# Optimization experiments

Measured on AMD Instinct MI355X. Metric: run time of the kernel, lower is better.

The kernel has to match this reference:

```python
import jax, jax.numpy as jnp
import numpy as np
from itertools import combinations_with_replacement

LATENT_DIM = 16
N_PARAMS = 2
N_VARS = LATENT_DIM + N_PARAMS  # 18
POLY_ORDER = 3
BATCH = 131072

# Static exponent index tables: for each degree d, an [n_terms_d, d] array of
# variable indices (combinations with replacement), matching a sympy-style
# polynomial library [1, x_i, x_i*x_j, x_i*x_j*x_k, ...].
IDX = [np.array(list(combinations_with_replacement(range(N_VARS), d)), dtype=np.int32)
       for d in range(1, POLY_ORDER + 1)]
P = 1 + sum(a.shape[0] for a in IDX)  # 1330 library terms


def setup_inputs() -> dict:
    key = jax.random.key(0)
    k1, k2, k3 = jax.random.split(key, 3)
    z = jax.random.normal(k1, (BATCH, LATENT_DIM), dtype=jnp.float32)
    betas = jax.random.normal(k2, (BATCH, N_PARAMS), dtype=jnp.float32)
    big_xi = jax.random.normal(k3, (P, N_VARS), dtype=jnp.float32) * 0.1
    mask = jnp.ones((P, N_VARS), dtype=jnp.float32)
    return {"z": z, "betas": betas, "big_xi": big_xi, "mask": mask}


def _theta(x):
    # x: [B, N_VARS] -> theta: [B, P]
    cols = [jnp.ones((x.shape[0], 1), dtype=x.dtype)]  # constant term
    for idx in IDX:
        acc = x[:, idx[:, 0]]                # [B, n_terms_d]
        for k in range(1, idx.shape[1]):     # loop over degree (<= POLY_ORDER)
            acc = acc * x[:, idx[:, k]]
        cols.append(acc)
    return jnp.concatenate(cols, axis=1)


def reference(z, betas, big_xi, mask):
    x = jnp.concatenate([z, betas], axis=1)  # [B, N_VARS]
    theta = _theta(x)                        # [B, P]
    return theta @ (big_xi * mask)           # [B, N_VARS]
```

## Files before the change

### kernel.cpp

```cpp
#include <hip/hip_runtime.h>
#include <hip/hip_bf16.h>
#include <utility>


constexpr int NVARS   = 18;
constexpr int NOUT    = 18;
constexpr int NROWS   = 131072;
constexpr int PTERMS  = 1330;
constexpr int NCHUNKS = 43;
constexpr int NSLOTS  = NCHUNKS * 8;

constexpr int WF0_SHORTS = NCHUNKS * 512;
constexpr int WF1_SHORTS = NCHUNKS * 64;
constexpr int WF_SHORTS  = WF0_SHORTS + WF1_SHORTS;

typedef __attribute__((ext_vector_type(8))) short short8;
typedef __attribute__((ext_vector_type(4))) float f32x4;

struct T3 { int a, b, c; };

constexpr int rho1(int v) {
    if (v < 16)  return (v & ~3) | ((v + 1) & 3);
    if (v == 16) return 17;
    if (v == 17) return 16;
    return v;
}
constexpr int rho2v(int v) { return rho1(rho1(v)); }

constexpr T3 sort3(int u0, int u1, int u2) {
    int t = 0;
    if (u0 > u1) { t = u0; u0 = u1; u1 = t; }
    if (u1 > u2) { t = u1; u1 = u2; u2 = t; }
    if (u0 > u1) { t = u0; u0 = u1; u1 = t; }
    return T3{u0, u1, u2};
}
constexpr T3 rho3(T3 t) { return sort3(rho1(t.a), rho1(t.b), rho1(t.c)); }

constexpr bool t3_less(T3 x, T3 y) {
    if (x.a != y.a) return x.a < y.a;
    if (x.b != y.b) return x.b < y.b;
    return x.c < y.c;
}
constexpr bool t3_eq(T3 x, T3 y) { return x.a == y.a && x.b == y.b && x.c == y.c; }

constexpr int rank_of(T3 t) {
    int deg = (t.a < 18) + (t.b < 18) + (t.c < 18);
    if (deg == 0) return 0;
    if (deg == 1) return 1 + t.a;
    if (deg == 2) {
        int r = 19;
        for (int a = 0; a < t.a; ++a) r += 18 - a;
        return r + (t.b - t.a);
    }
    int r = 190;
    for (int a = 0; a < t.a; ++a) { int n = 18 - a; r += n * (n + 1) / 2; }
    for (int b = t.a; b < t.b; ++b) r += 18 - b;
    return r + (t.c - t.b);
}

struct RepTables {
    signed char va[NSLOTS], vb[NSLOTS], vc[NSLOTS];
    short p[4][NSLOTS];
    int count;
};

constexpr void consider(RepTables& R, int& s, T3 t) {
    T3 im[4] = {t, T3{0, 0, 0}, T3{0, 0, 0}, T3{0, 0, 0}};
    im[1] = rho3(im[0]);
    im[2] = rho3(im[1]);
    im[3] = rho3(im[2]);
    for (int g = 1; g < 4; ++g)
        if (t3_less(im[g], t)) return;
    R.va[s] = (signed char)t.a; R.vb[s] = (signed char)t.b; R.vc[s] = (signed char)t.c;
    for (int g = 0; g < 4; ++g) {
        bool dup = false;
        for (int h = 0; h < g; ++h)
            if (t3_eq(im[h], im[g])) dup = true;
        R.p[g][s] = dup ? (short)-1 : (short)rank_of(im[g]);
    }
    ++s;
}

constexpr RepTables make_tables() {
    RepTables R{};
    int s = 0;
    consider(R, s, T3{18, 18, 18});
    for (int a = 0; a < NVARS; ++a) consider(R, s, T3{a, 18, 18});
    for (int a = 0; a < NVARS; ++a)
        for (int b = a; b < NVARS; ++b) consider(R, s, T3{a, b, 18});
    for (int a = 0; a < NVARS; ++a)
        for (int b = a; b < NVARS; ++b)
            for (int c = b; c < NVARS; ++c) consider(R, s, T3{a, b, c});
    R.count = s;
    for (; s < NSLOTS; ++s) {
        R.va[s] = 19; R.vb[s] = 19; R.vc[s] = 19;
        for (int g = 0; g < 4; ++g) R.p[g][s] = -1;
    }
    return R;
}

constexpr RepTables h_tab = make_tables();
static_assert(h_tab.count == 342, "orbit enumeration must give 342 rep slots");
__device__ const RepTables d_tab = make_tables();


#if __has_builtin(__builtin_amdgcn_cvt_pk_bf16_f32)
typedef __bf16 bf16x2 __attribute__((ext_vector_type(2)));
__device__ __forceinline__ unsigned pack2(float f0, float f1) {
    bf16x2 r = __builtin_amdgcn_cvt_pk_bf16_f32(f0, f1);
    return __builtin_bit_cast(unsigned, r);
}
#else
__device__ __forceinline__ unsigned pack2(float f0, float f1) {
    unsigned u0 = __float_as_uint(f0) + 0x8000u;
    unsigned u1 = __float_as_uint(f1) + 0x8000u;
    return __builtin_amdgcn_perm(u1, u0, 0x07060302u);
}
#endif


template <int S>
__device__ __forceinline__ float term_val(const float (&x)[NVARS]) {
    constexpr int a = h_tab.va[S], b = h_tab.vb[S], c = h_tab.vc[S];
    if constexpr (a >= 19)      return 0.0f;
    else if constexpr (a == 18) return 1.0f;
    else if constexpr (b == 18) return x[a];
    else if constexpr (c == 18) return x[a] * x[b];
    else                        return x[a] * x[b] * x[c];
}

union AFrag { unsigned u[4]; short8 v; };
union BFrag { unsigned u[4]; short8 v; };

template <int CI, int... I>
__device__ __forceinline__ void eval8(const float (&x)[NVARS], float (&t)[8],
                                      std::integer_sequence<int, I...>) {
    ((t[I] = term_val<CI * 8 + I>(x)), ...);
}

template <int CI>
__device__ __forceinline__ void kstep(const float (&xA)[NVARS], const float (&xB)[NVARS],
                                      const short* p0, const short* p1, unsigned zmask,
                                      f32x4& acc00, f32x4& acc01,
                                      f32x4& acc10, f32x4& acc11) {
    float tA[8], tB[8];
    eval8<CI>(xA, tA, std::make_integer_sequence<int, 8>{});
    eval8<CI>(xB, tB, std::make_integer_sequence<int, 8>{});
    AFrag afA, afB;
#pragma unroll
    for (int j = 0; j < 4; ++j) {
        afA.u[j] = pack2(tA[2 * j], tA[2 * j + 1]);
        afB.u[j] = pack2(tB[2 * j], tB[2 * j + 1]);
    }
    short8 b0 = *(const short8*)(p0 + CI * 512);
    BFrag b1;
    b1.v = *(const short8*)(p1 + CI * 64);
#pragma unroll
    for (int j = 0; j < 4; ++j) b1.u[j] &= zmask;
    acc00 = __builtin_amdgcn_mfma_f32_16x16x32_bf16(afA.v, b0,   acc00, 0, 0, 0);
    acc10 = __builtin_amdgcn_mfma_f32_16x16x32_bf16(afB.v, b0,   acc10, 0, 0, 0);
    acc01 = __builtin_amdgcn_mfma_f32_16x16x32_bf16(afA.v, b1.v, acc01, 0, 0, 0);
    acc11 = __builtin_amdgcn_mfma_f32_16x16x32_bf16(afB.v, b1.v, acc11, 0, 0, 0);
}

template <int... CI>
__device__ __forceinline__ void kloop(const float (&xA)[NVARS], const float (&xB)[NVARS],
                                      const short* p0, const short* p1, unsigned zmask,
                                      f32x4& acc00, f32x4& acc01,
                                      f32x4& acc10, f32x4& acc11,
                                      std::integer_sequence<int, CI...>) {
    (kstep<CI>(xA, xB, p0, p1, zmask, acc00, acc01, acc10, acc11), ...);
}

__device__ __forceinline__ void load_x(const float* __restrict__ z,
                                       const float* __restrict__ betas,
                                       int arow, bool s1, bool s2, float (&x)[NVARS]) {
    float x0[NVARS];
    const float4* z4 = (const float4*)(z + (size_t)arow * 16);
    float4 v0 = z4[0], v1 = z4[1], v2 = z4[2], v3 = z4[3];
    x0[0]  = v0.x; x0[1]  = v0.y; x0[2]  = v0.z; x0[3]  = v0.w;
    x0[4]  = v1.x; x0[5]  = v1.y; x0[6]  = v1.z; x0[7]  = v1.w;
    x0[8]  = v2.x; x0[9]  = v2.y; x0[10] = v2.z; x0[11] = v2.w;
    x0[12] = v3.x; x0[13] = v3.y; x0[14] = v3.z; x0[15] = v3.w;
    const float2 b2 = *(const float2*)(betas + (size_t)arow * 2);
    x0[16] = b2.x; x0[17] = b2.y;
    float y[NVARS];
#pragma unroll
    for (int v = 0; v < NVARS; ++v) y[v] = s1 ? x0[rho1(v)] : x0[v];
#pragma unroll
    for (int v = 0; v < NVARS; ++v) x[v] = s2 ? y[rho2v(v)] : y[v];
}

__global__ __launch_bounds__(256, 4) void vindy_mfma(const float* __restrict__ z,
                                                     const float* __restrict__ betas,
                                                     const short* __restrict__ wf,
                                                     float* __restrict__ out) {
    __shared__ __align__(16) short ldsW[WF_SHORTS];
    {
        const float4* src = (const float4*)wf;
        float4* dst = (float4*)ldsW;
        for (int i = threadIdx.x; i < WF_SHORTS / 8; i += 256) dst[i] = src[i];
    }
    __syncthreads();

    const int lane = threadIdx.x & 63;
    const int wave = threadIdx.x >> 6;
    const int g    = lane >> 4;
    const int n    = lane & 15;
    const int rowbase = blockIdx.x * 128 + wave * 32;

    const bool s1 = (g & 1) != 0;
    const bool s2 = (g & 2) != 0;
    float xA[NVARS], xB[NVARS];
    load_x(z, betas, rowbase + n,      s1, s2, xA);
    load_x(z, betas, rowbase + 16 + n, s1, s2, xB);

    const unsigned zmask = (n < 2) ? 0xFFFFFFFFu : 0u;
    const short* p0 = ldsW + lane * 8;
    const short* p1 = ldsW + WF0_SHORTS + (g * 2 + (n < 2 ? n : 0)) * 8;

    f32x4 acc00, acc01, acc10, acc11;
#pragma unroll
    for (int i = 0; i < 4; ++i) { acc00[i] = 0.0f; acc01[i] = 0.0f; acc10[i] = 0.0f; acc11[i] = 0.0f; }

    kloop(xA, xB, p0, p1, zmask, acc00, acc01, acc10, acc11,
          std::make_integer_sequence<int, NCHUNKS>{});

    float* o0 = out + (size_t)(rowbase + g * 4) * NOUT;
    float* o1 = out + (size_t)(rowbase + 16 + g * 4) * NOUT;
#pragma unroll
    for (int r = 0; r < 4; ++r) {
        o0[(size_t)r * NOUT + n] = acc00[r];
        o1[(size_t)r * NOUT + n] = acc10[r];
    }
    if (n < 2) {
#pragma unroll
        for (int r = 0; r < 4; ++r) {
            o0[(size_t)r * NOUT + 16 + n] = acc01[r];
            o1[(size_t)r * NOUT + 16 + n] = acc11[r];
        }
    }
}


__global__ void prep_wfrag(const float* __restrict__ xi, const float* __restrict__ mask,
                           __hip_bfloat16* __restrict__ wf) {
    int i = blockIdx.x * blockDim.x + threadIdx.x;
    if (i >= WF_SHORTS) return;
    int p = -1, col = 0;
    if (i < WF0_SHORTS) {
        int j = i & 7, l = (i >> 3) & 63, c = i >> 9;
        col = l & 15;
        p = d_tab.p[l >> 4][c * 8 + j];
    } else {
        int i2 = i - WF0_SHORTS;
        int j = i2 & 7, q = (i2 >> 3) & 7, c = i2 >> 6;
        col = 16 + (q & 1);
        p = d_tab.p[q >> 1][c * 8 + j];
    }
    float v = 0.0f;
    if (p >= 0) v = xi[p * NOUT + col] * mask[p * NOUT + col];
    wf[i] = __float2bfloat16(v);
}

extern "C" void kernel_launch(void* const* d_in, const int* in_sizes, int n_in,
                              void* d_out, int out_size, void* d_ws, size_t ws_size,
                              hipStream_t stream) {
    const float* z     = (const float*)d_in[0];
    const float* betas = (const float*)d_in[1];
    const float* xi    = (const float*)d_in[2];
    const float* mask  = (const float*)d_in[3];
    __hip_bfloat16* wf = (__hip_bfloat16*)d_ws;
    float* out = (float*)d_out;

    prep_wfrag<<<(WF_SHORTS + 255) / 256, 256, 0, stream>>>(xi, mask, wf);
    vindy_mfma<<<NROWS / 128, 256, 0, stream>>>(z, betas, (const short*)d_ws, out);
}
```

Baseline: 90.45 us.

## Use 1024-thread blocks and zero-padded B1 fragment slots instead of masking

Measured after the change: 96.91 us. +7.1%, slower.

```diff
diff --git a/kernel.cpp b/kernel.cpp
--- a/kernel.cpp
+++ b/kernel.cpp
@@ -11,7 +11,7 @@
 constexpr int NSLOTS  = NCHUNKS * 8;
 
 constexpr int WF0_SHORTS = NCHUNKS * 512;
-constexpr int WF1_SHORTS = NCHUNKS * 64;
+constexpr int WF1_SHORTS = NCHUNKS * 12 * 8;
 constexpr int WF_SHORTS  = WF0_SHORTS + WF1_SHORTS;
 
 typedef __attribute__((ext_vector_type(8))) short short8;
@@ -130,7 +130,6 @@
 }
 
 union AFrag { unsigned u[4]; short8 v; };
-union BFrag { unsigned u[4]; short8 v; };
 
 template <int CI, int... I>
 __device__ __forceinline__ void eval8(const float (&x)[NVARS], float (&t)[8],
@@ -140,7 +139,7 @@
 
 template <int CI>
 __device__ __forceinline__ void kstep(const float (&xA)[NVARS], const float (&xB)[NVARS],
-                                      const short* p0, const short* p1, unsigned zmask,
+                                      const short* p0, const short* p1,
                                       f32x4& acc00, f32x4& acc01,
                                       f32x4& acc10, f32x4& acc11) {
     float tA[8], tB[8];
@@ -153,23 +152,20 @@
         afB.u[j] = pack2(tB[2 * j], tB[2 * j + 1]);
     }
     short8 b0 = *(const short8*)(p0 + CI * 512);
-    BFrag b1;
-    b1.v = *(const short8*)(p1 + CI * 64);
-#pragma unroll
-    for (int j = 0; j < 4; ++j) b1.u[j] &= zmask;
-    acc00 = __builtin_amdgcn_mfma_f32_16x16x32_bf16(afA.v, b0,   acc00, 0, 0, 0);
-    acc10 = __builtin_amdgcn_mfma_f32_16x16x32_bf16(afB.v, b0,   acc10, 0, 0, 0);
-    acc01 = __builtin_amdgcn_mfma_f32_16x16x32_bf16(afA.v, b1.v, acc01, 0, 0, 0);
-    acc11 = __builtin_amdgcn_mfma_f32_16x16x32_bf16(afB.v, b1.v, acc11, 0, 0, 0);
+    short8 b1 = *(const short8*)(p1 + CI * (12 * 8));
+    acc00 = __builtin_amdgcn_mfma_f32_16x16x32_bf16(afA.v, b0, acc00, 0, 0, 0);
+    acc10 = __builtin_amdgcn_mfma_f32_16x16x32_bf16(afB.v, b0, acc10, 0, 0, 0);
+    acc01 = __builtin_amdgcn_mfma_f32_16x16x32_bf16(afA.v, b1, acc01, 0, 0, 0);
+    acc11 = __builtin_amdgcn_mfma_f32_16x16x32_bf16(afB.v, b1, acc11, 0, 0, 0);
 }
 
 template <int... CI>
 __device__ __forceinline__ void kloop(const float (&xA)[NVARS], const float (&xB)[NVARS],
-                                      const short* p0, const short* p1, unsigned zmask,
+                                      const short* p0, const short* p1,
                                       f32x4& acc00, f32x4& acc01,
                                       f32x4& acc10, f32x4& acc11,
                                       std::integer_sequence<int, CI...>) {
-    (kstep<CI>(xA, xB, p0, p1, zmask, acc00, acc01, acc10, acc11), ...);
+    (kstep<CI>(xA, xB, p0, p1, acc00, acc01, acc10, acc11), ...);
 }
 
 __device__ __forceinline__ void load_x(const float* __restrict__ z,
@@ -191,15 +187,15 @@
     for (int v = 0; v < NVARS; ++v) x[v] = s2 ? y[rho2v(v)] : y[v];
 }
 
-__global__ __launch_bounds__(256, 4) void vindy_mfma(const float* __restrict__ z,
-                                                     const float* __restrict__ betas,
-                                                     const short* __restrict__ wf,
-                                                     float* __restrict__ out) {
+__global__ __launch_bounds__(1024, 4) void vindy_mfma(const float* __restrict__ z,
+                                                      const float* __restrict__ betas,
+                                                      const short* __restrict__ wf,
+                                                      float* __restrict__ out) {
     __shared__ __align__(16) short ldsW[WF_SHORTS];
     {
         const float4* src = (const float4*)wf;
         float4* dst = (float4*)ldsW;
-        for (int i = threadIdx.x; i < WF_SHORTS / 8; i += 256) dst[i] = src[i];
+        for (int i = threadIdx.x; i < WF_SHORTS / 8; i += 1024) dst[i] = src[i];
     }
     __syncthreads();
 
@@ -207,7 +203,7 @@
     const int wave = threadIdx.x >> 6;
     const int g    = lane >> 4;
     const int n    = lane & 15;
-    const int rowbase = blockIdx.x * 128 + wave * 32;
+    const int rowbase = blockIdx.x * 512 + wave * 32;
 
     const bool s1 = (g & 1) != 0;
     const bool s2 = (g & 2) != 0;
@@ -215,15 +211,14 @@
     load_x(z, betas, rowbase + n,      s1, s2, xA);
     load_x(z, betas, rowbase + 16 + n, s1, s2, xB);
 
-    const unsigned zmask = (n < 2) ? 0xFFFFFFFFu : 0u;
     const short* p0 = ldsW + lane * 8;
-    const short* p1 = ldsW + WF0_SHORTS + (g * 2 + (n < 2 ? n : 0)) * 8;
+    const short* p1 = ldsW + WF0_SHORTS + (g * 3 + (n < 2 ? n : 2)) * 8;
 
     f32x4 acc00, acc01, acc10, acc11;
 #pragma unroll
     for (int i = 0; i < 4; ++i) { acc00[i] = 0.0f; acc01[i] = 0.0f; acc10[i] = 0.0f; acc11[i] = 0.0f; }
 
-    kloop(xA, xB, p0, p1, zmask, acc00, acc01, acc10, acc11,
+    kloop(xA, xB, p0, p1, acc00, acc01, acc10, acc11,
           std::make_integer_sequence<int, NCHUNKS>{});
 
     float* o0 = out + (size_t)(rowbase + g * 4) * NOUT;
@@ -254,9 +249,14 @@
         p = d_tab.p[l >> 4][c * 8 + j];
     } else {
         int i2 = i - WF0_SHORTS;
-        int j = i2 & 7, q = (i2 >> 3) & 7, c = i2 >> 6;
-        col = 16 + (q & 1);
-        p = d_tab.p[q >> 1][c * 8 + j];
+        int j = i2 & 7;
+        int q = (i2 >> 3) % 12;
+        int c = i2 / 96;
+        int qq = q % 3, gg = q / 3;
+        if (qq < 2) {
+            col = 16 + qq;
+            p = d_tab.p[gg][c * 8 + j];
+        }
     }
     float v = 0.0f;
     if (p >= 0) v = xi[p * NOUT + col] * mask[p * NOUT + col];
@@ -274,5 +274,5 @@
     float* out = (float*)d_out;
 
     prep_wfrag<<<(WF_SHORTS + 255) / 256, 256, 0, stream>>>(xi, mask, wf);
-    vindy_mfma<<<NROWS / 128, 256, 0, stream>>>(z, betas, (const short*)d_ws, out);
-}
+    vindy_mfma<<<NROWS / 512, 1024, 0, stream>>>(z, betas, (const short*)d_ws, out);
+}
```
